# Kernel optimization log

Hardware: AMD Instinct MI355X
Metric: run time of the kernel (lower is better)

The kernel has to match this reference:

```python
import jax, jax.numpy as jnp
import numpy as np

H = 8  # num_heads
C = 512  # embed_dims
L = 3  # num_layers
SCALE = (C // H) ** -0.5


def _ln(x, g, b, eps=1e-5):
    mu = jnp.mean(x, axis=-1, keepdims=True)
    var = jnp.mean((x - mu) ** 2, axis=-1, keepdims=True)
    return g * (x - mu) / jnp.sqrt(var + eps) + b


def setup_inputs() -> dict:
    key = jax.random.key(0)
    ks = jax.random.split(key, 12)
    B, Nq, Nk = 16, 64, 4096
    s = 0.02
    return dict(
        queries=jax.random.normal(ks[0], (B, Nq, C), jnp.float32),
        feat=jax.random.normal(ks[1], (B, Nk, C), jnp.float32),
        extra_token=jax.random.normal(ks[2], (B, 1, C), jnp.float32),
        Wq=jax.random.normal(ks[3], (L, C, C), jnp.float32) * s,
        bq=jnp.zeros((L, C), jnp.float32),
        Wk=jax.random.normal(ks[4], (L, C, C), jnp.float32) * s,
        bk=jnp.zeros((L, C), jnp.float32),
        Wv=jax.random.normal(ks[5], (L, C, C), jnp.float32) * s,
        bv=jnp.zeros((L, C), jnp.float32),
        Wo=jax.random.normal(ks[6], (L, C, C), jnp.float32) * s,
        bo=jnp.zeros((L, C), jnp.float32),
        W1=jax.random.normal(ks[7], (L, C, 4 * C), jnp.float32) * s,
        b1=jnp.zeros((L, 4 * C), jnp.float32),
        W2=jax.random.normal(ks[8], (L, 4 * C, C), jnp.float32) * s,
        b2=jnp.zeros((L, C), jnp.float32),
        g2=jnp.ones((L, C), jnp.float32),
        beta2=jnp.zeros((L, C), jnp.float32),
        g3=jnp.ones((L, C), jnp.float32),
        beta3=jnp.zeros((L, C), jnp.float32),
    )


def reference(queries, feat, extra_token, Wq, bq, Wk, bk, Wv, bv, Wo, bo,
              W1, b1, W2, b2, g2, beta2, g3, beta3):
    B, Nq, _ = queries.shape
    Nk = feat.shape[1]
    hd = C // H
    # extra gating token is NOT projected through q: raw reshape -> [B,H,1,hd]
    eq = extra_token.reshape(B, 1, H, hd).transpose(0, 2, 1, 3)
    x = queries
    outs, attns, affs = [], [], []
    for i in range(L):
        q = (x @ Wq[i] + bq[i]).reshape(B, Nq, H, hd).transpose(0, 2, 1, 3)
        k = (feat @ Wk[i] + bk[i]).reshape(B, Nk, H, hd).transpose(0, 2, 1, 3)
        v = (feat @ Wv[i] + bv[i]).reshape(B, Nk, H, hd).transpose(0, 2, 1, 3)
        attn = jnp.einsum('bhqd,bhkd->bhqk', q, k) * SCALE  # pre-softmax scores
        # affinity gate from extra token, averaged over heads -> [B,1,1,Nk]
        aff = jax.nn.sigmoid(jnp.mean(
            jnp.einsum('bhod,bhkd->bhok', eq, k) * SCALE, axis=1, keepdims=True))
        p = aff * jax.nn.softmax(attn, axis=-1)  # gated probabilities
        o = jnp.einsum('bhqk,bhkd->bqhd', p, v).reshape(B, Nq, C)
        o = o @ Wo[i] + bo[i]
        x = _ln(x + o, g2[i], beta2[i])
        ff = jax.nn.relu(x @ W1[i] + b1[i]) @ W2[i] + b2[i]
        x = _ln(x + ff, g3[i], beta3[i])
        outs.append(x)
        attns.append(attn.sum(axis=1) / H)  # head-averaged pre-softmax scores
        affs.append(aff)
    return (jnp.stack(outs), jnp.stack(attns), jnp.stack(affs))
```

## Files before the change

kernel.cpp:

```cpp
#include <hip/hip_runtime.h>


typedef unsigned short u16;
typedef __attribute__((ext_vector_type(8))) short short8;
typedef __attribute__((ext_vector_type(4))) short short4v;
typedef __attribute__((ext_vector_type(4))) float f32x4;

__device__ __forceinline__ float b2f(u16 u) {
    union { unsigned int i; float f; } v; v.i = ((unsigned int)u) << 16; return v.f;
}
__device__ __forceinline__ u16 f2b(float f) {
    unsigned int x = __float_as_uint(f);
    x += 0x7fffu + ((x >> 16) & 1u);
    return (u16)(x >> 16);
}

__device__ __forceinline__ float waveSum(float v) {
#pragma unroll
    for (int o = 32; o > 0; o >>= 1) v += __shfl_xor(v, o);
    return v;
}

__device__ __forceinline__ void gl_lds16(const void* g, void* l) {
    __builtin_amdgcn_global_load_lds(
        (__attribute__((address_space(1))) void*)g,
        (__attribute__((address_space(3))) void*)l, 16, 0, 0);
}

template<bool BIAS_ROW, bool HAS_BIAS, bool AFFC>
__global__ __launch_bounds__(512, 1) void gemm256v3_k(
    const u16* __restrict__ A, const u16* __restrict__ Bt,
    const float* __restrict__ bias, u16* __restrict__ Cout,
    int lda, int ldb, int ldc, long sA2, long sB2, long sC2,
    const float* __restrict__ affc)
{
    __shared__ u16 Ah[4][256][32];
    __shared__ u16 Bh[4][256][32];
    const int tid = threadIdx.x;
    const int lane = tid & 63;
    const int wave = tid >> 6;

    const int gx = gridDim.x, gy = gridDim.y;
    const int nwg = gx * gy * gridDim.z;
    int id;
    {
        const int orig = blockIdx.x + blockIdx.y * gx + blockIdx.z * gx * gy;
        const int qq = nwg >> 3, rr = nwg & 7;
        const int xcd = orig & 7, sub = orig >> 3;
        id = (xcd < rr ? xcd * (qq + 1) : rr * (qq + 1) + (xcd - rr) * qq) + sub;
    }
    const int bx = id % gx;
    const int by = (id / gx) % gy;
    const int z  = id / (gx * gy);

    A  += (long)z * sA2;
    Bt += (long)z * sB2;
    const long cbase = (long)z * sC2;
    const int n0 = bx * 256;
    const int m0 = by * 256;
    const int wm = wave >> 2;
    const int wn = wave & 3;
    const int rl = lane & 15;
    const int uq = lane >> 4;
    const int srow = lane >> 2;
    const int up   = lane & 3;

    f32x4 acc[8][4];
#pragma unroll
    for (int i = 0; i < 8; ++i)
#pragma unroll
        for (int j = 0; j < 4; ++j) acc[i][j] = (f32x4){0.f, 0.f, 0.f, 0.f};

    auto stage_round = [&](int h, int r) {
        const int slot = h & 3;
        const int k0 = h * 32;
        if (r < 2) {
            const int row = r * 128 + wave * 16 + srow;
            const int ul = up ^ ((row >> 2) & 3);
            gl_lds16(A + (long)(m0 + row) * lda + k0 + ul * 8,
                     &Ah[slot][r * 128 + wave * 16][0]);
        } else {
            const int row = (r - 2) * 128 + wave * 16 + srow;
            const int ul = up ^ ((row >> 2) & 3);
            gl_lds16(Bt + (long)(n0 + row) * ldb + k0 + ul * 8,
                     &Bh[slot][(r - 2) * 128 + wave * 16][0]);
        }
    };
    auto read_af = [&](int slot, int base, short8* dst) {
#pragma unroll
        for (int i = 0; i < 4; ++i) {
            const int R = wm * 128 + (base + i) * 16 + rl;
            dst[i] = *(const short8*)(&Ah[slot][R][(uq ^ ((R >> 2) & 3)) * 8]);
        }
    };
    auto read_bf = [&](int slot, short8* dst) {
#pragma unroll
        for (int j = 0; j < 4; ++j) {
            const int R = wn * 64 + j * 16 + rl;
            dst[j] = *(const short8*)(&Bh[slot][R][(uq ^ ((R >> 2) & 3)) * 8]);
        }
    };

#pragma unroll
    for (int h = 0; h < 3; ++h)
#pragma unroll
        for (int r = 0; r < 4; ++r) stage_round(h, r);
    asm volatile("s_waitcnt vmcnt(8)\n\ts_barrier" ::: "memory");

    short8 afA[4], afB[4], bfC[4], afN[4], bfN[4];
    read_bf(0, bfC);
    read_af(0, 0, afA);

#pragma unroll
    for (int h = 0; h < 16; ++h) {
        const int slot = h & 3;
        if (h + 3 < 16) { stage_round(h + 3, 0); stage_round(h + 3, 1); }
        read_af(slot, 4, afB);
        __builtin_amdgcn_s_setprio(1);
#pragma unroll
        for (int i = 0; i < 4; ++i)
#pragma unroll
            for (int j = 0; j < 4; ++j)
                acc[i][j] = __builtin_amdgcn_mfma_f32_16x16x32_bf16(
                    afA[i], bfC[j], acc[i][j], 0, 0, 0);
        __builtin_amdgcn_s_setprio(0);

        if (h + 3 < 16) { stage_round(h + 3, 2); stage_round(h + 3, 3); }
        if (h < 13)
            asm volatile("s_waitcnt vmcnt(8)\n\ts_barrier" ::: "memory");
        else if (h == 13)
            asm volatile("s_waitcnt vmcnt(4)\n\ts_barrier" ::: "memory");
        else if (h == 14)
            asm volatile("s_waitcnt vmcnt(0)\n\ts_barrier" ::: "memory");
        if (h < 15) {
            read_bf((h + 1) & 3, bfN);
            read_af((h + 1) & 3, 0, afN);
        }
        __builtin_amdgcn_s_setprio(1);
#pragma unroll
        for (int i = 0; i < 4; ++i)
#pragma unroll
            for (int j = 0; j < 4; ++j)
                acc[4 + i][j] = __builtin_amdgcn_mfma_f32_16x16x32_bf16(
                    afB[i], bfC[j], acc[4 + i][j], 0, 0, 0);
        __builtin_amdgcn_s_setprio(0);
        if (h < 15) {
#pragma unroll
            for (int i = 0; i < 4; ++i) { afA[i] = afN[i]; bfC[i] = bfN[i]; }
        }
    }

    const int r0 = (lane >> 4) * 4;
    const int c0 = lane & 15;
#pragma unroll
    for (int i = 0; i < 8; ++i) {
#pragma unroll
        for (int j = 0; j < 4; ++j) {
#pragma unroll
            for (int r = 0; r < 4; ++r) {
                const int row = m0 + wm * 128 + i * 16 + r0 + r;
                const int col = n0 + wn * 64 + j * 16 + c0;
                float v = acc[i][j][r];
                if constexpr (HAS_BIAS) {
                    if constexpr (BIAS_ROW) v += bias[row]; else v += bias[col];
                }
                if constexpr (AFFC) v *= affc[(long)z * 4096 + col];
                Cout[cbase + (long)row * ldc + col] = f2b(v);
            }
        }
    }
}

__global__ __launch_bounds__(256) void fattn_k(
    const u16* __restrict__ q16, const u16* __restrict__ K16,
    const u16* __restrict__ VT16, float* __restrict__ Op,
    float2* __restrict__ ml)
{
    __shared__ u16 Qs[64][64];
    __shared__ u16 Ks[128][64];
    __shared__ u16 Vs[64][128];
    __shared__ u16 Ps[64][128];
    const int t = threadIdx.x;
    const int lane = t & 63;
    const int w = t >> 6;
    const int bh = blockIdx.y;
    const int split = blockIdx.x;
    const int b = bh >> 3, h = bh & 7;
    const int kbase = split * 1024;
    const int rl = lane & 15, uq = lane >> 4;
    const int r0 = (lane >> 4) * 4;
    const int c0 = lane & 15;
    const int srow8 = lane >> 3, up8 = lane & 7;
    const int srow4 = lane >> 4, up16 = lane & 15;

#pragma unroll
    for (int rnd = 0; rnd < 2; ++rnd) {
        const int row = rnd * 32 + w * 8 + srow8;
        const int ul = up8 ^ (row & 7);
        gl_lds16(q16 + ((long)(b * 64 + row)) * 512 + h * 64 + ul * 8,
                 &Qs[rnd * 32 + w * 8][0]);
    }

    f32x4 O[4];
#pragma unroll
    for (int n = 0; n < 4; ++n) O[n] = (f32x4){0.f, 0.f, 0.f, 0.f};
    float m_run[4] = {-3.0e38f, -3.0e38f, -3.0e38f, -3.0e38f};
    float l_run[4] = {0.f, 0.f, 0.f, 0.f};

    const int R = w * 16 + rl;

    for (int tt = 0; tt < 8; ++tt) {
        __syncthreads();
#pragma unroll
        for (int rnd = 0; rnd < 4; ++rnd) {
            const int row = rnd * 32 + w * 8 + srow8;
            const int ul = up8 ^ (row & 7);
            gl_lds16(K16 + ((long)(b * 4096 + kbase + tt * 128 + row)) * 512
                         + h * 64 + ul * 8,
                     &Ks[rnd * 32 + w * 8][0]);
        }
#pragma unroll
        for (int rnd = 0; rnd < 4; ++rnd) {
            const int row = rnd * 16 + w * 4 + srow4;
            const int ul = up16 ^ (row & 15);
            gl_lds16(VT16 + (long)b * 2097152 + ((long)(h * 64 + row)) * 4096
                         + kbase + tt * 128 + ul * 8,
                     &Vs[rnd * 16 + w * 4][0]);
        }
        __syncthreads();

        f32x4 s[8];
        short8 af[2];
#pragma unroll
        for (int kc = 0; kc < 2; ++kc)
            af[kc] = *(const short8*)(&Qs[R][((kc * 4 + uq) ^ (R & 7)) * 8]);
#pragma unroll
        for (int j = 0; j < 8; ++j) {
            s[j] = (f32x4){0.f, 0.f, 0.f, 0.f};
            const int Rb = j * 16 + rl;
#pragma unroll
            for (int kc = 0; kc < 2; ++kc) {
                short8 bf = *(const short8*)(&Ks[Rb][((kc * 4 + uq) ^ (Rb & 7)) * 8]);
                s[j] = __builtin_amdgcn_mfma_f32_16x16x32_bf16(af[kc], bf, s[j], 0, 0, 0);
            }
        }
#pragma unroll
        for (int j = 0; j < 8; ++j)
#pragma unroll
            for (int r = 0; r < 4; ++r) s[j][r] *= 0.125f;

        float mv[4];
#pragma unroll
        for (int r = 0; r < 4; ++r) {
            float m = s[0][r];
#pragma unroll
            for (int j = 1; j < 8; ++j) m = fmaxf(m, s[j][r]);
#pragma unroll
            for (int mask = 1; mask < 16; mask <<= 1)
                m = fmaxf(m, __shfl_xor(m, mask));
            mv[r] = m;
        }
        float al[4], rs[4];
#pragma unroll
        for (int r = 0; r < 4; ++r) {
            const float mn = fmaxf(m_run[r], mv[r]);
            al[r] = __expf(m_run[r] - mn);
            m_run[r] = mn;
            rs[r] = 0.f;
        }
#pragma unroll
        for (int j = 0; j < 8; ++j)
#pragma unroll
            for (int r = 0; r < 4; ++r) {
                s[j][r] = __expf(s[j][r] - m_run[r]);
                rs[r] += s[j][r];
            }
#pragma unroll
        for (int r = 0; r < 4; ++r) {
#pragma unroll
            for (int mask = 1; mask < 16; mask <<= 1)
                rs[r] += __shfl_xor(rs[r], mask);
            l_run[r] = l_run[r] * al[r] + rs[r];
        }
#pragma unroll
        for (int n = 0; n < 4; ++n)
#pragma unroll
            for (int r = 0; r < 4; ++r) O[n][r] *= al[r];

#pragma unroll
        for (int j = 0; j < 8; ++j)
#pragma unroll
            for (int r = 0; r < 4; ++r) {
                const int row = w * 16 + r0 + r;
                const int col = j * 16 + c0;
                Ps[row][(((col >> 3) ^ (row & 15)) << 3) + (col & 7)] = f2b(s[j][r]);
            }
#pragma unroll
        for (int kc4 = 0; kc4 < 4; ++kc4) {
            const short8 afp = *(const short8*)(&Ps[R][(((kc4 * 4 + uq) ^ (R & 15)) << 3)]);
#pragma unroll
            for (int n = 0; n < 4; ++n) {
                const int Rv = n * 16 + rl;
                const short8 bfv = *(const short8*)(&Vs[Rv][(((kc4 * 4 + uq) ^ (Rv & 15)) << 3)]);
                O[n] = __builtin_amdgcn_mfma_f32_16x16x32_bf16(afp, bfv, O[n], 0, 0, 0);
            }
        }
    }

    const long obase = ((long)(split * 128 + bh)) * 64;
#pragma unroll
    for (int n = 0; n < 4; ++n)
#pragma unroll
        for (int r = 0; r < 4; ++r) {
            const int q = w * 16 + r0 + r;
            Op[(obase + q) * 64 + n * 16 + c0] = O[n][r];
        }
    if (c0 == 0) {
#pragma unroll
        for (int r = 0; r < 4; ++r) {
            const int q = w * 16 + r0 + r;
            ml[obase + q] = make_float2(m_run[r], l_run[r]);
        }
    }
}

__global__ __launch_bounds__(256) void fmerge_k(
    const float* __restrict__ Op, const float2* __restrict__ ml,
    u16* __restrict__ o16)
{
    const int i = blockIdx.x * 256 + threadIdx.x;
    const int d4 = i & 15;
    const int q  = (i >> 4) & 63;
    const int bh = i >> 10;
    const float2 m0 = ml[((long)(0 * 128 + bh)) * 64 + q];
    const float2 m1 = ml[((long)(1 * 128 + bh)) * 64 + q];
    const float2 m2 = ml[((long)(2 * 128 + bh)) * 64 + q];
    const float2 m3 = ml[((long)(3 * 128 + bh)) * 64 + q];
    const float m = fmaxf(fmaxf(m0.x, m1.x), fmaxf(m2.x, m3.x));
    const float e0 = __expf(m0.x - m), e1 = __expf(m1.x - m);
    const float e2 = __expf(m2.x - m), e3 = __expf(m3.x - m);
    const float inv = 1.f / (m0.y * e0 + m1.y * e1 + m2.y * e2 + m3.y * e3);
    const float4 v0 = *(const float4*)(Op + (((long)(0 * 128 + bh)) * 64 + q) * 64 + d4 * 4);
    const float4 v1 = *(const float4*)(Op + (((long)(1 * 128 + bh)) * 64 + q) * 64 + d4 * 4);
    const float4 v2 = *(const float4*)(Op + (((long)(2 * 128 + bh)) * 64 + q) * 64 + d4 * 4);
    const float4 v3 = *(const float4*)(Op + (((long)(3 * 128 + bh)) * 64 + q) * 64 + d4 * 4);
    float4 acc;
    acc.x = (v0.x * e0 + v1.x * e1 + v2.x * e2 + v3.x * e3) * inv;
    acc.y = (v0.y * e0 + v1.y * e1 + v2.y * e2 + v3.y * e3) * inv;
    acc.z = (v0.z * e0 + v1.z * e1 + v2.z * e2 + v3.z * e3) * inv;
    acc.w = (v0.w * e0 + v1.w * e1 + v2.w * e2 + v3.w * e3) * inv;
    const int b = bh >> 3, h = bh & 7;
    short4v r;
    r[0] = (short)f2b(acc.x); r[1] = (short)f2b(acc.y);
    r[2] = (short)f2b(acc.z); r[3] = (short)f2b(acc.w);
    *(short4v*)(o16 + (long)b * 32768 + q * 512 + h * 64 + d4 * 4) = r;
}

template<int TM, int TN, bool OUT_BF16, bool RELU, bool BIAS_ROW, bool HAS_BIAS>
__global__ __launch_bounds__(256) void gemm_bt_k(
    const u16* __restrict__ A, const u16* __restrict__ Bt,
    const float* __restrict__ bias, void* __restrict__ Cout,
    int K, int lda, int ldb, int ldc,
    long sA1, long sB1, long sC1, float alpha)
{
    __shared__ u16 As[TM][64];
    __shared__ u16 Bs[TN][64];
    const int t = threadIdx.x;
    const int lane = t & 63;
    const int wave = t >> 6;
    const int z = blockIdx.z;
    A  += (long)z * sA1;
    Bt += (long)z * sB1;
    const long cbase = (long)z * sC1;
    const int n0 = blockIdx.x * TN;
    const int m0 = blockIdx.y * TM;
    constexpr int FM = TM / 32, FN = TN / 32;
    const int wr = wave >> 1, wc = wave & 1;
    const int rl = lane & 15, uq = lane >> 4;

    f32x4 acc[FM][FN];
#pragma unroll
    for (int i = 0; i < FM; ++i)
#pragma unroll
        for (int j = 0; j < FN; ++j) acc[i][j] = (f32x4){0.f, 0.f, 0.f, 0.f};

    const int srow = lane >> 3;
    const int up   = lane & 7;

    for (int k0 = 0; k0 < K; k0 += 64) {
        __syncthreads();
#pragma unroll
        for (int r = 0; r < TM / 32; ++r) {
            const int br = (wave * (TM / 32) + r) * 8;
            const int row = br + srow;
            const int ul = up ^ (row & 7);
            gl_lds16(A + (long)(m0 + row) * lda + k0 + ul * 8, &As[br][0]);
        }
#pragma unroll
        for (int r = 0; r < TN / 32; ++r) {
            const int br = (wave * (TN / 32) + r) * 8;
            const int row = br + srow;
            const int ul = up ^ (row & 7);
            gl_lds16(Bt + (long)(n0 + row) * ldb + k0 + ul * 8, &Bs[br][0]);
        }
        __syncthreads();

#pragma unroll
        for (int kc = 0; kc < 2; ++kc) {
            short8 af[FM], bf[FN];
#pragma unroll
            for (int i = 0; i < FM; ++i) {
                const int R = wr * (TM / 2) + i * 16 + rl;
                af[i] = *(const short8*)(&As[R][((kc * 4 + uq) ^ (R & 7)) * 8]);
            }
#pragma unroll
            for (int j = 0; j < FN; ++j) {
                const int R = wc * (TN / 2) + j * 16 + rl;
                bf[j] = *(const short8*)(&Bs[R][((kc * 4 + uq) ^ (R & 7)) * 8]);
            }
#pragma unroll
            for (int i = 0; i < FM; ++i)
#pragma unroll
                for (int j = 0; j < FN; ++j)
                    acc[i][j] = __builtin_amdgcn_mfma_f32_16x16x32_bf16(
                        af[i], bf[j], acc[i][j], 0, 0, 0);
        }
    }

    const int r0 = (lane >> 4) * 4;
    const int c0 = lane & 15;
#pragma unroll
    for (int i = 0; i < FM; ++i) {
#pragma unroll
        for (int j = 0; j < FN; ++j) {
#pragma unroll
            for (int r = 0; r < 4; ++r) {
                const int row = m0 + wr * (TM / 2) + i * 16 + r0 + r;
                const int col = n0 + wc * (TN / 2) + j * 16 + c0;
                float v = acc[i][j][r] * alpha;
                if constexpr (HAS_BIAS) {
                    if constexpr (BIAS_ROW) v += bias[row]; else v += bias[col];
                }
                if constexpr (RELU) v = fmaxf(v, 0.f);
                const long idx = cbase + (long)row * ldc + col;
                if constexpr (OUT_BF16) ((u16*)Cout)[idx] = f2b(v);
                else                    ((float*)Cout)[idx] = v;
            }
        }
    }
}

__global__ __launch_bounds__(256) void ffred_k(
    const float* __restrict__ part, const float* __restrict__ bias,
    float* __restrict__ out)
{
    const int i = (blockIdx.x * 256 + threadIdx.x) * 4;
    const int c = i & 511;
    float4 s = *(const float4*)(part + i);
#pragma unroll
    for (int sp = 1; sp < 4; ++sp) {
        const float4 v = *(const float4*)(part + (long)sp * 524288 + i);
        s.x += v.x; s.y += v.y; s.z += v.z; s.w += v.w;
    }
    s.x += bias[c]; s.y += bias[c + 1]; s.z += bias[c + 2]; s.w += bias[c + 3];
    *(float4*)(out + i) = s;
}

__global__ __launch_bounds__(256) void umat_k(
    const float* __restrict__ Wk, const float* __restrict__ extra,
    float* __restrict__ u)
{
    __shared__ float ex[16][512];
    const int l = blockIdx.x;
    const int t = threadIdx.x;
    for (int i = t; i < 16 * 512 / 4; i += 256)
        ((float4*)&ex[0][0])[i] = ((const float4*)extra)[i];
    __syncthreads();
    const int lane = t & 63, wave = t >> 6;
    const int row = blockIdx.y * 4 + wave;
    const float* wrow = Wk + ((size_t)l * 512 + row) * 512 + lane * 8;
    float w[8];
#pragma unroll
    for (int j = 0; j < 8; ++j) w[j] = wrow[j];
    float s[16];
#pragma unroll
    for (int b = 0; b < 16; ++b) {
        float x = 0.f;
#pragma unroll
        for (int j = 0; j < 8; ++j) x += w[j] * ex[b][lane * 8 + j];
        s[b] = waveSum(x);
    }
    if (lane < 16) u[((size_t)l * 16 + lane) * 512 + row] = s[lane];
}

__global__ __launch_bounds__(256) void cbk_k(
    const float* __restrict__ bk, const float* __restrict__ extra,
    float* __restrict__ cb)
{
    const int gw = blockIdx.x * 4 + (threadIdx.x >> 6);
    const int lane = threadIdx.x & 63;
    const int l = gw >> 4, b = gw & 15;
    float s = 0.f;
#pragma unroll
    for (int j = 0; j < 8; ++j)
        s += extra[b * 512 + lane * 8 + j] * bk[l * 512 + lane * 8 + j];
    s = waveSum(s);
    if (lane == 0) cb[gw] = s;
}

__global__ __launch_bounds__(256) void cvt16_aff_k(
    const float* __restrict__ feat, u16* __restrict__ dst,
    const float* __restrict__ u, const float* __restrict__ cb,
    float* __restrict__ affb, float* __restrict__ affs_out)
{
    const int t = blockIdx.x * 256 + threadIdx.x;
    const long i = (long)t * 8;
    const int lane = threadIdx.x & 63;
    const int r = t >> 6;
    const int b = r >> 12;
    const float4 a0 = *(const float4*)(feat + i);
    const float4 a1 = *(const float4*)(feat + i + 4);
    short8 o;
    o[0] = (short)f2b(a0.x); o[1] = (short)f2b(a0.y);
    o[2] = (short)f2b(a0.z); o[3] = (short)f2b(a0.w);
    o[4] = (short)f2b(a1.x); o[5] = (short)f2b(a1.y);
    o[6] = (short)f2b(a1.z); o[7] = (short)f2b(a1.w);
    *(short8*)(dst + i) = o;
    const float f[8] = {a0.x, a0.y, a0.z, a0.w, a1.x, a1.y, a1.z, a1.w};
#pragma unroll
    for (int l = 0; l < 3; ++l) {
        const float* ur = u + ((size_t)l * 16 + b) * 512 + lane * 8;
        float s = 0.f;
#pragma unroll
        for (int j = 0; j < 8; ++j) s += f[j] * ur[j];
        s = waveSum(s);
        if (lane == 0) {
            const float av = 1.f / (1.f + __expf(-0.015625f * (s + cb[l * 16 + b])));
            affb[l * 65536 + r] = av;
            affs_out[l * 65536 + r] = av;
        }
    }
}

template<bool WRITE_OUT>
__global__ __launch_bounds__(256) void ln_k(
    float* __restrict__ x, const float* __restrict__ add,
    const float* __restrict__ g, const float* __restrict__ be,
    u16* __restrict__ x16, float* __restrict__ outp)
{
    const int r = blockIdx.x, t = threadIdx.x;
    const int w = t >> 6, lane = t & 63;
    __shared__ float red[4];
    float* xr = x + (long)r * 512;
    const float* ar = add + (long)r * 512;
    const float v0 = xr[2 * t]     + ar[2 * t];
    const float v1 = xr[2 * t + 1] + ar[2 * t + 1];
    float s = waveSum(v0 + v1);
    if (lane == 0) red[w] = s;
    __syncthreads();
    s = red[0] + red[1] + red[2] + red[3];
    const float mu = s * (1.f / 512.f);
    const float d0 = v0 - mu, d1 = v1 - mu;
    __syncthreads();
    float vs = waveSum(d0 * d0 + d1 * d1);
    if (lane == 0) red[w] = vs;
    __syncthreads();
    vs = red[0] + red[1] + red[2] + red[3];
    const float rs = rsqrtf(vs * (1.f / 512.f) + 1e-5f);
    const float o0 = g[2 * t]     * d0 * rs + be[2 * t];
    const float o1 = g[2 * t + 1] * d1 * rs + be[2 * t + 1];
    xr[2 * t] = o0; xr[2 * t + 1] = o1;
    x16[(long)r * 512 + 2 * t]     = f2b(o0);
    x16[(long)r * 512 + 2 * t + 1] = f2b(o1);
    if constexpr (WRITE_OUT) {
        outp[(long)r * 512 + 2 * t]     = o0;
        outp[(long)r * 512 + 2 * t + 1] = o1;
    }
}

__global__ __launch_bounds__(256) void initx_k(
    const float* __restrict__ src, float* __restrict__ x, u16* __restrict__ x16)
{
    const long i = ((long)blockIdx.x * 256 + threadIdx.x) * 8;
    const float4 a = *(const float4*)(src + i);
    const float4 b = *(const float4*)(src + i + 4);
    *(float4*)(x + i) = a;
    *(float4*)(x + i + 4) = b;
    short8 r;
    r[0] = (short)f2b(a.x); r[1] = (short)f2b(a.y); r[2] = (short)f2b(a.z); r[3] = (short)f2b(a.w);
    r[4] = (short)f2b(b.x); r[5] = (short)f2b(b.y); r[6] = (short)f2b(b.z); r[7] = (short)f2b(b.w);
    *(short8*)(x16 + i) = r;
}

__global__ __launch_bounds__(256) void transpose_w_k(
    const float* __restrict__ W, u16* __restrict__ WT, int K, int N)
{
    __shared__ float tile[32][33];
    const int z = blockIdx.z;
    W  += (size_t)z * K * N;
    WT += (size_t)z * K * N;
    const int n0 = blockIdx.x * 32, k0 = blockIdx.y * 32;
    const int tx = threadIdx.x & 31, ty = threadIdx.x >> 5;
#pragma unroll
    for (int j = 0; j < 32; j += 8)
        tile[ty + j][tx] = W[(size_t)(k0 + ty + j) * N + n0 + tx];
    __syncthreads();
#pragma unroll
    for (int j = 0; j < 32; j += 8)
        WT[(size_t)(n0 + ty + j) * K + k0 + tx] = f2b(tile[tx][ty + j]);
}

extern "C" void kernel_launch(void* const* d_in, const int* in_sizes, int n_in,
                              void* d_out, int out_size, void* d_ws, size_t ws_size,
                              hipStream_t stream)
{
    (void)in_sizes; (void)n_in; (void)out_size; (void)ws_size;
    const float* queries = (const float*)d_in[0];
    const float* feat    = (const float*)d_in[1];
    const float* extra   = (const float*)d_in[2];
    const float* Wq = (const float*)d_in[3];  const float* bq = (const float*)d_in[4];
    const float* Wk = (const float*)d_in[5];  const float* bk = (const float*)d_in[6];
    const float* Wv = (const float*)d_in[7];  const float* bv = (const float*)d_in[8];
    const float* Wo = (const float*)d_in[9];  const float* bo = (const float*)d_in[10];
    const float* W1 = (const float*)d_in[11]; const float* b1 = (const float*)d_in[12];
    const float* W2 = (const float*)d_in[13]; const float* b2 = (const float*)d_in[14];
    const float* g2 = (const float*)d_in[15]; const float* be2 = (const float*)d_in[16];
    const float* g3 = (const float*)d_in[17]; const float* be3 = (const float*)d_in[18];

    char* wsb = (char*)d_ws;
    size_t off = 0;
    auto alloc = [&](size_t bytes) -> char* {
        char* p = wsb + off; off += (bytes + 255) & ~(size_t)255; return p;
    };
    u16*  feat16 = (u16*)alloc(33554432ull * 2);
    u16*  WqT = (u16*)alloc(786432ull * 2);
    u16*  WkT = (u16*)alloc(786432ull * 2);
    u16*  WvT = (u16*)alloc(786432ull * 2);
    u16*  WoT = (u16*)alloc(786432ull * 2);
    u16*  W1T = (u16*)alloc(3145728ull * 2);
    u16*  W2T = (u16*)alloc(3145728ull * 2);
    u16*  K16 = (u16*)alloc(33554432ull * 2);
    u16*  VT16 = (u16*)alloc(33554432ull * 2);
    u16*  q16 = (u16*)alloc(524288ull * 2);
    float* Op  = (float*)alloc(4194304ull * 4);
    float2* ml = (float2*)alloc(32768ull * 8);
    float* affb  = (float*)alloc(196608ull * 4);
    u16*  o16 = (u16*)alloc(524288ull * 2);
    float* oproj = (float*)alloc(524288ull * 4);
    float* xb    = (float*)alloc(524288ull * 4);
    u16*  x16 = (u16*)alloc(524288ull * 2);
    u16*  h116 = (u16*)alloc(2097152ull * 2);
    float* ffb   = (float*)alloc(524288ull * 4);
    float* uvec  = (float*)alloc(24576ull * 4);
    float* cb    = (float*)alloc(48ull * 4);
    float* part2 = (float*)VT16;

    float* out_f = (float*)d_out;
    float* outs_base  = out_f;
    float* attns_base = out_f + 1572864;
    float* affs_base  = out_f + 14155776;

    umat_k<<<dim3(3, 128), 256, 0, stream>>>(Wk, extra, uvec);
    cbk_k<<<12, 256, 0, stream>>>(bk, extra, cb);
    cvt16_aff_k<<<16384, 256, 0, stream>>>(feat, feat16, uvec, cb, affb, affs_base);
    initx_k<<<256, 256, 0, stream>>>(queries, xb, x16);
    transpose_w_k<<<dim3(16, 16, 3), 256, 0, stream>>>(Wq, WqT, 512, 512);
    transpose_w_k<<<dim3(16, 16, 3), 256, 0, stream>>>(Wk, WkT, 512, 512);
    transpose_w_k<<<dim3(16, 16, 3), 256, 0, stream>>>(Wv, WvT, 512, 512);
    transpose_w_k<<<dim3(16, 16, 3), 256, 0, stream>>>(Wo, WoT, 512, 512);
    transpose_w_k<<<dim3(64, 16, 3), 256, 0, stream>>>(W1, W1T, 512, 2048);
    transpose_w_k<<<dim3(16, 64, 3), 256, 0, stream>>>(W2, W2T, 2048, 512);

    for (int i = 0; i < 3; ++i) {
        gemm256v3_k<false, true, false><<<dim3(2, 256, 1), 512, 0, stream>>>(
            feat16, WkT + i * 262144, bk + i * 512, K16,
            512, 512, 512, 0, 0, 0, nullptr);
        gemm256v3_k<true, true, true><<<dim3(16, 2, 16), 512, 0, stream>>>(
            WvT + i * 262144, feat16, bv + i * 512, VT16,
            512, 512, 4096, 0, 2097152, 2097152, affb + i * 65536);
        gemm_bt_k<64, 64, true, false, false, true>
            <<<dim3(8, 16, 1), 256, 0, stream>>>(
            x16, WqT + i * 262144, bq + i * 512, q16,
            512, 512, 512, 512, 0, 0, 0, 1.f);
        gemm_bt_k<64, 128, false, false, false, false>
            <<<dim3(32, 1, 16), 256, 0, stream>>>(
            q16, K16, nullptr, attns_base + (size_t)i * 4194304,
            512, 512, 512, 4096, 32768, 2097152, 262144, 0.015625f);
        fattn_k<<<dim3(4, 128), 256, 0, stream>>>(q16, K16, VT16, Op, ml);
        fmerge_k<<<512, 256, 0, stream>>>(Op, ml, o16);
        gemm_bt_k<64, 64, false, false, false, true>
            <<<dim3(8, 16, 1), 256, 0, stream>>>(
            o16, WoT + i * 262144, bo + i * 512, oproj,
            512, 512, 512, 512, 0, 0, 0, 1.f);
        ln_k<false><<<1024, 256, 0, stream>>>(xb, oproj, g2 + i * 512, be2 + i * 512, x16, nullptr);
        gemm_bt_k<64, 128, true, true, false, true>
            <<<dim3(16, 16, 1), 256, 0, stream>>>(
            x16, W1T + (size_t)i * 1048576, b1 + i * 2048, h116,
            512, 512, 512, 2048, 0, 0, 0, 1.f);
        gemm_bt_k<64, 64, false, false, false, false>
            <<<dim3(8, 16, 4), 256, 0, stream>>>(
            h116, W2T + (size_t)i * 1048576, nullptr, part2,
            512, 2048, 2048, 512, 512, 512, 524288, 1.f);
        ffred_k<<<512, 256, 0, stream>>>(part2, b2 + i * 512, ffb);
        ln_k<true><<<1024, 256, 0, stream>>>(xb, ffb, g3 + i * 512, be3 + i * 512, x16,
                                             outs_base + (size_t)i * 524288);
    }
}
```

Measured before the change: 658.0 us.

## Batch K/V projections for all layers into single launches and fuse split-K reduce with LayerNorm

When the workspace is large enough, the K and V projection GEMMs for all three layers run as one launch each, with per-layer strides added to the GEMM kernel, and their results are stored in triple-sized buffers. This replaces six small launches and gives better occupancy, since the K GEMM with 512 blocks becomes 1536 blocks. The FFN split-K reduction and bias add are fused into the final LayerNorm kernel, which removes one kernel and one intermediate round trip. The cost is much larger workspace use, and the split-K partials now alias the Op buffer.

Result: no change. 663.6 us (+0.8%).

```diff
diff --git a/kernel.cpp b/kernel.cpp
--- a/kernel.cpp
+++ b/kernel.cpp
@@ -31,7 +31,8 @@
 __global__ __launch_bounds__(512, 1) void gemm256v3_k(
     const u16* __restrict__ A, const u16* __restrict__ Bt,
     const float* __restrict__ bias, u16* __restrict__ Cout,
-    int lda, int ldb, int ldc, long sA2, long sB2, long sC2,
+    int lda, int ldb, int ldc, int bdiv,
+    long sA1, long sA2, long sB1, long sB2, long sC1, long sC2,
     const float* __restrict__ affc)
 {
     __shared__ u16 Ah[4][256][32];
@@ -52,10 +53,12 @@
     const int bx = id % gx;
     const int by = (id / gx) % gy;
     const int z  = id / (gx * gy);
-
-    A  += (long)z * sA2;
-    Bt += (long)z * sB2;
-    const long cbase = (long)z * sC2;
+    const int zq = z / bdiv, zr = z % bdiv;
+
+    A  += zq * sA1 + zr * sA2;
+    Bt += zq * sB1 + zr * sB2;
+    const long cbase = (long)zq * sC1 + (long)zr * sC2;
+    const float* biasp = bias + zq * 512;
     const int n0 = bx * 256;
     const int m0 = by * 256;
     const int wm = wave >> 2;
@@ -162,9 +165,10 @@
                 const int col = n0 + wn * 64 + j * 16 + c0;
                 float v = acc[i][j][r];
                 if constexpr (HAS_BIAS) {
-                    if constexpr (BIAS_ROW) v += bias[row]; else v += bias[col];
+                    if constexpr (BIAS_ROW) v += biasp[row]; else v += biasp[col];
                 }
-                if constexpr (AFFC) v *= affc[(long)z * 4096 + col];
+                if constexpr (AFFC)
+                    v *= affc[(long)zq * 65536 + (long)zr * 4096 + col];
                 Cout[cbase + (long)row * ldc + col] = f2b(v);
             }
         }
@@ -450,103 +454,49 @@
     }
 }
 
-__global__ __launch_bounds__(256) void ffred_k(
-    const float* __restrict__ part, const float* __restrict__ bias,
-    float* __restrict__ out)
-{
-    const int i = (blockIdx.x * 256 + threadIdx.x) * 4;
-    const int c = i & 511;
-    float4 s = *(const float4*)(part + i);
-#pragma unroll
-    for (int sp = 1; sp < 4; ++sp) {
-        const float4 v = *(const float4*)(part + (long)sp * 524288 + i);
-        s.x += v.x; s.y += v.y; s.z += v.z; s.w += v.w;
-    }
-    s.x += bias[c]; s.y += bias[c + 1]; s.z += bias[c + 2]; s.w += bias[c + 3];
-    *(float4*)(out + i) = s;
-}
-
-__global__ __launch_bounds__(256) void umat_k(
-    const float* __restrict__ Wk, const float* __restrict__ extra,
-    float* __restrict__ u)
-{
-    __shared__ float ex[16][512];
-    const int l = blockIdx.x;
-    const int t = threadIdx.x;
-    for (int i = t; i < 16 * 512 / 4; i += 256)
-        ((float4*)&ex[0][0])[i] = ((const float4*)extra)[i];
+__global__ __launch_bounds__(256) void ffln_k(
+    const float* __restrict__ part, const float* __restrict__ b2,
+    float* __restrict__ x, const float* __restrict__ g,
+    const float* __restrict__ be, u16* __restrict__ x16,
+    float* __restrict__ outp)
+{
+    const int r = blockIdx.x, t = threadIdx.x;
+    const int w = t >> 6, lane = t & 63;
+    __shared__ float red[4];
+    const long idx0 = (long)r * 512 + 2 * t;
+    float f0 = 0.f, f1 = 0.f;
+#pragma unroll
+    for (int sp = 0; sp < 4; ++sp) {
+        const float2 v = *(const float2*)(part + (long)sp * 524288 + idx0);
+        f0 += v.x; f1 += v.y;
+    }
+    f0 += b2[2 * t]; f1 += b2[2 * t + 1];
+    float* xr = x + (long)r * 512;
+    const float v0 = xr[2 * t]     + f0;
+    const float v1 = xr[2 * t + 1] + f1;
+    float s = waveSum(v0 + v1);
+    if (lane == 0) red[w] = s;
     __syncthreads();
-    const int lane = t & 63, wave = t >> 6;
-    const int row = blockIdx.y * 4 + wave;
-    const float* wrow = Wk + ((size_t)l * 512 + row) * 512 + lane * 8;
-    float w[8];
-#pragma unroll
-    for (int j = 0; j < 8; ++j) w[j] = wrow[j];
-    float s[16];
-#pragma unroll
-    for (int b = 0; b < 16; ++b) {
-        float x = 0.f;
-#pragma unroll
-        for (int j = 0; j < 8; ++j) x += w[j] * ex[b][lane * 8 + j];
-        s[b] = waveSum(x);
-    }
-    if (lane < 16) u[((size_t)l * 16 + lane) * 512 + row] = s[lane];
-}
-
-__global__ __launch_bounds__(256) void cbk_k(
-    const float* __restrict__ bk, const float* __restrict__ extra,
-    float* __restrict__ cb)
-{
-    const int gw = blockIdx.x * 4 + (threadIdx.x >> 6);
-    const int lane = threadIdx.x & 63;
-    const int l = gw >> 4, b = gw & 15;
-    float s = 0.f;
-#pragma unroll
-    for (int j = 0; j < 8; ++j)
-        s += extra[b * 512 + lane * 8 + j] * bk[l * 512 + lane * 8 + j];
-    s = waveSum(s);
-    if (lane == 0) cb[gw] = s;
-}
-
-__global__ __launch_bounds__(256) void cvt16_aff_k(
-    const float* __restrict__ feat, u16* __restrict__ dst,
-    const float* __restrict__ u, const float* __restrict__ cb,
-    float* __restrict__ affb, float* __restrict__ affs_out)
-{
-    const int t = blockIdx.x * 256 + threadIdx.x;
-    const long i = (long)t * 8;
-    const int lane = threadIdx.x & 63;
-    const int r = t >> 6;
-    const int b = r >> 12;
-    const float4 a0 = *(const float4*)(feat + i);
-    const float4 a1 = *(const float4*)(feat + i + 4);
-    short8 o;
-    o[0] = (short)f2b(a0.x); o[1] = (short)f2b(a0.y);
-    o[2] = (short)f2b(a0.z); o[3] = (short)f2b(a0.w);
-    o[4] = (short)f2b(a1.x); o[5] = (short)f2b(a1.y);
-    o[6] = (short)f2b(a1.z); o[7] = (short)f2b(a1.w);
-    *(short8*)(dst + i) = o;
-    const float f[8] = {a0.x, a0.y, a0.z, a0.w, a1.x, a1.y, a1.z, a1.w};
-#pragma unroll
-    for (int l = 0; l < 3; ++l) {
-        const float* ur = u + ((size_t)l * 16 + b) * 512 + lane * 8;
-        float s = 0.f;
-#pragma unroll
-        for (int j = 0; j < 8; ++j) s += f[j] * ur[j];
-        s = waveSum(s);
-        if (lane == 0) {
-            const float av = 1.f / (1.f + __expf(-0.015625f * (s + cb[l * 16 + b])));
-            affb[l * 65536 + r] = av;
-            affs_out[l * 65536 + r] = av;
-        }
-    }
-}
-
-template<bool WRITE_OUT>
+    s = red[0] + red[1] + red[2] + red[3];
+    const float mu = s * (1.f / 512.f);
+    const float d0 = v0 - mu, d1 = v1 - mu;
+    __syncthreads();
+    float vs = waveSum(d0 * d0 + d1 * d1);
+    if (lane == 0) red[w] = vs;
+    __syncthreads();
+    vs = red[0] + red[1] + red[2] + red[3];
+    const float rs = rsqrtf(vs * (1.f / 512.f) + 1e-5f);
+    const float o0 = g[2 * t]     * d0 * rs + be[2 * t];
+    const float o1 = g[2 * t + 1] * d1 * rs + be[2 * t + 1];
+    xr[2 * t] = o0; xr[2 * t + 1] = o1;
+    x16[idx0] = f2b(o0); x16[idx0 + 1] = f2b(o1);
+    outp[idx0] = o0; outp[idx0 + 1] = o1;
+}
+
 __global__ __launch_bounds__(256) void ln_k(
     float* __restrict__ x, const float* __restrict__ add,
     const float* __restrict__ g, const float* __restrict__ be,
-    u16* __restrict__ x16, float* __restrict__ outp)
+    u16* __restrict__ x16)
 {
     const int r = blockIdx.x, t = threadIdx.x;
     const int w = t >> 6, lane = t & 63;
@@ -572,9 +522,81 @@
     xr[2 * t] = o0; xr[2 * t + 1] = o1;
     x16[(long)r * 512 + 2 * t]     = f2b(o0);
     x16[(long)r * 512 + 2 * t + 1] = f2b(o1);
-    if constexpr (WRITE_OUT) {
-        outp[(long)r * 512 + 2 * t]     = o0;
-        outp[(long)r * 512 + 2 * t + 1] = o1;
+}
+
+__global__ __launch_bounds__(256) void umat_k(
+    const float* __restrict__ Wk, const float* __restrict__ extra,
+    float* __restrict__ u)
+{
+    __shared__ float ex[16][512];
+    const int l = blockIdx.x;
+    const int t = threadIdx.x;
+    for (int i = t; i < 16 * 512 / 4; i += 256)
+        ((float4*)&ex[0][0])[i] = ((const float4*)extra)[i];
+    __syncthreads();
+    const int lane = t & 63, wave = t >> 6;
+    const int row = blockIdx.y * 4 + wave;
+    const float* wrow = Wk + ((size_t)l * 512 + row) * 512 + lane * 8;
+    float w[8];
+#pragma unroll
+    for (int j = 0; j < 8; ++j) w[j] = wrow[j];
+    float s[16];
+#pragma unroll
+    for (int b = 0; b < 16; ++b) {
+        float x = 0.f;
+#pragma unroll
+        for (int j = 0; j < 8; ++j) x += w[j] * ex[b][lane * 8 + j];
+        s[b] = waveSum(x);
+    }
+    if (lane < 16) u[((size_t)l * 16 + lane) * 512 + row] = s[lane];
+}
+
+__global__ __launch_bounds__(256) void cbk_k(
+    const float* __restrict__ bk, const float* __restrict__ extra,
+    float* __restrict__ cb)
+{
+    const int gw = blockIdx.x * 4 + (threadIdx.x >> 6);
+    const int lane = threadIdx.x & 63;
+    const int l = gw >> 4, b = gw & 15;
+    float s = 0.f;
+#pragma unroll
+    for (int j = 0; j < 8; ++j)
+        s += extra[b * 512 + lane * 8 + j] * bk[l * 512 + lane * 8 + j];
+    s = waveSum(s);
+    if (lane == 0) cb[gw] = s;
+}
+
+__global__ __launch_bounds__(256) void cvt16_aff_k(
+    const float* __restrict__ feat, u16* __restrict__ dst,
+    const float* __restrict__ u, const float* __restrict__ cb,
+    float* __restrict__ affb, float* __restrict__ affs_out)
+{
+    const int t = blockIdx.x * 256 + threadIdx.x;
+    const long i = (long)t * 8;
+    const int lane = threadIdx.x & 63;
+    const int r = t >> 6;
+    const int b = r >> 12;
+    const float4 a0 = *(const float4*)(feat + i);
+    const float4 a1 = *(const float4*)(feat + i + 4);
+    short8 o;
+    o[0] = (short)f2b(a0.x); o[1] = (short)f2b(a0.y);
+    o[2] = (short)f2b(a0.z); o[3] = (short)f2b(a0.w);
+    o[4] = (short)f2b(a1.x); o[5] = (short)f2b(a1.y);
+    o[6] = (short)f2b(a1.z); o[7] = (short)f2b(a1.w);
+    *(short8*)(dst + i) = o;
+    const float f[8] = {a0.x, a0.y, a0.z, a0.w, a1.x, a1.y, a1.z, a1.w};
+#pragma unroll
+    for (int l = 0; l < 3; ++l) {
+        const float* ur = u + ((size_t)l * 16 + b) * 512 + lane * 8;
+        float s = 0.f;
+#pragma unroll
+        for (int j = 0; j < 8; ++j) s += f[j] * ur[j];
+        s = waveSum(s);
+        if (lane == 0) {
+            const float av = 1.f / (1.f + __expf(-0.015625f * (s + cb[l * 16 + b])));
+            affb[l * 65536 + r] = av;
+            affs_out[l * 65536 + r] = av;
+        }
     }
 }
 
@@ -614,7 +636,7 @@
                               void* d_out, int out_size, void* d_ws, size_t ws_size,
                               hipStream_t stream)
 {
-    (void)in_sizes; (void)n_in; (void)out_size; (void)ws_size;
+    (void)in_sizes; (void)n_in; (void)out_size;
     const float* queries = (const float*)d_in[0];
     const float* feat    = (const float*)d_in[1];
     const float* extra   = (const float*)d_in[2];
@@ -626,6 +648,9 @@
     const float* W2 = (const float*)d_in[13]; const float* b2 = (const float*)d_in[14];
     const float* g2 = (const float*)d_in[15]; const float* be2 = (const float*)d_in[16];
     const float* g3 = (const float*)d_in[17]; const float* be3 = (const float*)d_in[18];
+
+    const bool big = ws_size >= 520000000ull;
+    const long KL = big ? 33554432L : 0L;
 
     char* wsb = (char*)d_ws;
     size_t off = 0;
@@ -639,8 +664,8 @@
     u16*  WoT = (u16*)alloc(786432ull * 2);
     u16*  W1T = (u16*)alloc(3145728ull * 2);
     u16*  W2T = (u16*)alloc(3145728ull * 2);
-    u16*  K16 = (u16*)alloc(33554432ull * 2);
-    u16*  VT16 = (u16*)alloc(33554432ull * 2);
+    u16*  K16 = (u16*)alloc((big ? 3 : 1) * 33554432ull * 2);
+    u16*  VT16 = (u16*)alloc((big ? 3 : 1) * 33554432ull * 2);
     u16*  q16 = (u16*)alloc(524288ull * 2);
     float* Op  = (float*)alloc(4194304ull * 4);
     float2* ml = (float2*)alloc(32768ull * 8);
@@ -650,10 +675,9 @@
     float* xb    = (float*)alloc(524288ull * 4);
     u16*  x16 = (u16*)alloc(524288ull * 2);
     u16*  h116 = (u16*)alloc(2097152ull * 2);
-    float* ffb   = (float*)alloc(524288ull * 4);
     float* uvec  = (float*)alloc(24576ull * 4);
     float* cb    = (float*)alloc(48ull * 4);
-    float* part2 = (float*)VT16;
+    float* part2 = Op;
 
     float* out_f = (float*)d_out;
     float* outs_base  = out_f;
@@ -671,28 +695,41 @@
     transpose_w_k<<<dim3(64, 16, 3), 256, 0, stream>>>(W1, W1T, 512, 2048);
     transpose_w_k<<<dim3(16, 64, 3), 256, 0, stream>>>(W2, W2T, 2048, 512);
 
+    if (big) {
+        gemm256v3_k<false, true, false><<<dim3(2, 256, 3), 512, 0, stream>>>(
+            feat16, WkT, bk, K16, 512, 512, 512, 1,
+            0, 0, 262144, 0, 33554432, 0, nullptr);
+        gemm256v3_k<true, true, true><<<dim3(16, 2, 48), 512, 0, stream>>>(
+            WvT, feat16, bv, VT16, 512, 512, 4096, 16,
+            262144, 0, 0, 2097152, 33554432, 2097152, affb);
+    }
+
     for (int i = 0; i < 3; ++i) {
-        gemm256v3_k<false, true, false><<<dim3(2, 256, 1), 512, 0, stream>>>(
-            feat16, WkT + i * 262144, bk + i * 512, K16,
-            512, 512, 512, 0, 0, 0, nullptr);
-        gemm256v3_k<true, true, true><<<dim3(16, 2, 16), 512, 0, stream>>>(
-            WvT + i * 262144, feat16, bv + i * 512, VT16,
-            512, 512, 4096, 0, 2097152, 2097152, affb + i * 65536);
+        if (!big) {
+            gemm256v3_k<false, true, false><<<dim3(2, 256, 1), 512, 0, stream>>>(
+                feat16, WkT + i * 262144, bk + i * 512, K16, 512, 512, 512, 1,
+                0, 0, 0, 0, 0, 0, nullptr);
+            gemm256v3_k<true, true, true><<<dim3(16, 2, 16), 512, 0, stream>>>(
+                WvT + i * 262144, feat16, bv + i * 512, VT16, 512, 512, 4096, 16,
+                0, 0, 0, 2097152, 0, 2097152, affb + i * 65536);
+        }
+        const u16* Ki = K16 + (size_t)i * KL;
+        const u16* Vi = VT16 + (size_t)i * KL;
         gemm_bt_k<64, 64, true, false, false, true>
             <<<dim3(8, 16, 1), 256, 0, stream>>>(
             x16, WqT + i * 262144, bq + i * 512, q16,
             512, 512, 512, 512, 0, 0, 0, 1.f);
         gemm_bt_k<64, 128, false, false, false, false>
             <<<dim3(32, 1, 16), 256, 0, stream>>>(
-            q16, K16, nullptr, attns_base + (size_t)i * 4194304,
+            q16, Ki, nullptr, attns_base + (size_t)i * 4194304,
             512, 512, 512, 4096, 32768, 2097152, 262144, 0.015625f);
-        fattn_k<<<dim3(4, 128), 256, 0, stream>>>(q16, K16, VT16, Op, ml);
+        fattn_k<<<dim3(4, 128), 256, 0, stream>>>(q16, Ki, Vi, Op, ml);
         fmerge_k<<<512, 256, 0, stream>>>(Op, ml, o16);
         gemm_bt_k<64, 64, false, false, false, true>
             <<<dim3(8, 16, 1), 256, 0, stream>>>(
             o16, WoT + i * 262144, bo + i * 512, oproj,
             512, 512, 512, 512, 0, 0, 0, 1.f);
-        ln_k<false><<<1024, 256, 0, stream>>>(xb, oproj, g2 + i * 512, be2 + i * 512, x16, nullptr);
+        ln_k<<<1024, 256, 0, stream>>>(xb, oproj, g2 + i * 512, be2 + i * 512, x16);
         gemm_bt_k<64, 128, true, true, false, true>
             <<<dim3(16, 16, 1), 256, 0, stream>>>(
             x16, W1T + (size_t)i * 1048576, b1 + i * 2048, h116,
@@ -701,8 +738,8 @@
             <<<dim3(8, 16, 4), 256, 0, stream>>>(
             h116, W2T + (size_t)i * 1048576, nullptr, part2,
             512, 2048, 2048, 512, 512, 512, 524288, 1.f);
-        ffred_k<<<512, 256, 0, stream>>>(part2, b2 + i * 512, ffb);
-        ln_k<true><<<1024, 256, 0, stream>>>(xb, ffb, g3 + i * 512, be3 + i * 512, x16,
-                                             outs_base + (size_t)i * 524288);
-    }
-}
+        ffln_k<<<1024, 256, 0, stream>>>(part2, b2 + i * 512, xb,
+                                         g3 + i * 512, be3 + i * 512, x16,
+                                         outs_base + (size_t)i * 524288);
+    }
+}
```
